# Kernel tuning notes

Measured on AMD Instinct MI355X. Metric: run time of the kernel, lower is better.

## Reference

```python
import jax, jax.numpy as jnp
import numpy as np

B, L, D, H, HD = 2, 8192, 1024, 16, 64
MINI = 64
NC = L // MINI
TTT_BASE_LR = 1.0
NUM_CHUNKS = 4
TEXT_LEN = 64
INIT_OFFSET = 2048


def setup_inputs() -> dict:
    key = jax.random.key(0)
    ks = jax.random.split(key, 16)
    hidden_states = jax.random.normal(ks[0], (B, L, D), dtype=jnp.float32)
    # llama-style rope table as (cos, sin) pairs: [L, HD//2, 2]
    inv_freq = 1.0 / (10000.0 ** (np.arange(0, HD, 2, dtype=np.float32) / HD))
    t = np.arange(L, dtype=np.float32)
    ang = np.outer(t, inv_freq)  # [L, HD//2]
    freqs_cis = jnp.asarray(np.stack([np.cos(ang), np.sin(ang)], axis=-1))
    std = 0.02
    inp = {"hidden_states": hidden_states, "freqs_cis": freqs_cis}
    names = ["wq", "wk", "wv", "wu"]
    for i, n in enumerate(names):
        inp[n + "_w"] = jax.random.normal(ks[1 + i], (D, D), dtype=jnp.float32) * std  # [in, out]
        inp[n + "_b"] = jnp.zeros((D,), dtype=jnp.float32)
    inp["ttt_norm_weight"] = jnp.ones((H, HD), dtype=jnp.float32)
    inp["ttt_norm_bias"] = jnp.zeros((H, HD), dtype=jnp.float32)
    inp["lr_weight"] = jax.random.normal(ks[6], (H, 1, D), dtype=jnp.float32) * std
    inp["lr_bias"] = jnp.zeros((H, 1), dtype=jnp.float32)
    return inp


def _l2norm(x):
    return x / jnp.maximum(jnp.linalg.norm(x, axis=-1, keepdims=True), 1e-12)


def _rope(x, cos, sin):
    # x: [B, L, H, HD]; cos/sin: [L, HD//2] -> broadcast [1, L, 1, HD//2]
    c = cos[None, :, None, :]
    s = sin[None, :, None, :]
    xr, xi = x[..., 0::2], x[..., 1::2]
    out_r = xr * c - xi * s
    out_i = xr * s + xi * c
    return jnp.stack([out_r, out_i], axis=-1).reshape(x.shape)


def _interleave(x):
    # x: [B, H, NC, C, F]; splice text chunks into video scenes (static offsets)
    b, h, nc, c, f = x.shape
    xf = x.reshape(b, h, nc * c, f)
    stl = TEXT_LEN * NUM_CHUNKS
    x_text = xf[:, :, :stl]
    x_video = xf[:, :, stl:]
    texts = jnp.split(x_text, NUM_CHUNKS, axis=2)
    vio = INIT_OFFSET - TEXT_LEN
    vids = [x_video[:, :, :vio]] + list(jnp.split(x_video[:, :, vio:], NUM_CHUNKS - 1, axis=2))
    pieces = [jnp.concatenate([texts[i], vids[i]], axis=2) for i in range(NUM_CHUNKS)]
    return jnp.concatenate(pieces, axis=2).reshape(b, h, nc, c, f)


def reference(hidden_states, freqs_cis, wq_w, wq_b, wk_w, wk_b, wv_w, wv_b,
              wu_w, wu_b, ttt_norm_weight, ttt_norm_bias, lr_weight, lr_bias):
    X = hidden_states  # [B, L, D]
    XQ = (X @ wq_w + wq_b).reshape(B, L, H, HD)
    XK = (X @ wk_w + wk_b).reshape(B, L, H, HD)
    XV = (X @ wv_w + wv_b).reshape(B, L, H, HD)
    XU = (X @ wu_w + wu_b).reshape(B, L, H, HD)

    XQ, XK, XU = _l2norm(XQ), _l2norm(XK), _l2norm(XU)

    # seq_text_length = 0 in process_input -> rope over the whole sequence
    cos, sin = freqs_cis[..., 0], freqs_cis[..., 1]
    XQ = _rope(XQ, cos, sin)
    XK = _rope(XK, cos, sin)
    XU = _rope(XU, cos, sin)

    # ln reconstruction target (std uses Bessel correction like torch.std)
    diff = XV - XK
    mean = diff.mean(axis=-1, keepdims=True)
    std = jnp.std(diff, axis=-1, keepdims=True, ddof=1)
    norm = (diff - mean) / (std + 1e-8)
    XV = ttt_norm_weight[None, None] * norm + ttt_norm_bias[None, None] + XK

    # reshape to mini-batches: [B, H, NC, C, HD]
    def to_mb(t):
        return t.transpose(0, 2, 1, 3).reshape(B, H, NC, MINI, HD)
    XQ, XK, XV, XU = to_mb(XQ), to_mb(XK), to_mb(XV), to_mb(XU)
    Xmb = X.reshape(B, NC, MINI, D)

    # per-head LR gating
    ttt_lr = jnp.einsum('bnkc,hdc->bhnkd', Xmb, lr_weight) + lr_bias.reshape(1, -1, 1, 1, 1)
    ttt_lr = jax.nn.sigmoid(ttt_lr).transpose(0, 1, 2, 4, 3)  # [B, H, NC, 1, C]
    ttt_lr = TTT_BASE_LR * ttt_lr / HD
    eta = (1.0 / MINI) * jnp.tile(ttt_lr, (1, 1, 1, MINI, 1))  # [B, H, NC, C, C]

    XQ, XK, XV, XU = _interleave(XQ), _interleave(XK), _interleave(XV), _interleave(XU)
    eta = _interleave(eta)

    # HD == MINI == 64 so all five stack cleanly
    return jnp.stack([XQ, XK, XV, XU, eta], axis=0)
```

## Files before the change

kernel.cpp:

```cpp
#include <hip/hip_runtime.h>

typedef unsigned int u32;
typedef unsigned short u16;
typedef short short8v __attribute__((ext_vector_type(8)));
typedef float f32x4 __attribute__((ext_vector_type(4)));

#define ND 1024
#define NH 16
#define OUT_T ((size_t)16777216)

#define SBAR() __builtin_amdgcn_s_barrier()
#define VMW(n) asm volatile("s_waitcnt vmcnt(" #n ")" ::: "memory")
#define LGKM0() asm volatile("s_waitcnt lgkmcnt(0)" ::: "memory")

__device__ __forceinline__ u16 f2bf(float f) {
  u32 u = __float_as_uint(f);
  u32 r = u + 0x7fffu + ((u >> 16) & 1u);
  return (u16)(r >> 16);
}

__device__ __forceinline__ short8v pack8(float4 a, float4 b) {
  short8v v;
  v[0] = (short)f2bf(a.x); v[1] = (short)f2bf(a.y);
  v[2] = (short)f2bf(a.z); v[3] = (short)f2bf(a.w);
  v[4] = (short)f2bf(b.x); v[5] = (short)f2bf(b.y);
  v[6] = (short)f2bf(b.z); v[7] = (short)f2bf(b.w);
  return v;
}

__device__ __forceinline__ void gload16(const void* g, void* l) {
  __builtin_amdgcn_global_load_lds((const __attribute__((address_space(1))) void*)g,
                                   (__attribute__((address_space(3))) void*)l, 16, 0, 0);
}

__global__ void k_wt(const float* __restrict__ w0, const float* __restrict__ w1,
                     const float* __restrict__ w2, const float* __restrict__ w3,
                     u16* __restrict__ WT) {
  __shared__ float T[64][65];
  int bid = blockIdx.x;
  int w = bid >> 8;
  int tk = (bid >> 4) & 15, tc = bid & 15;
  const float* W = w == 0 ? w0 : w == 1 ? w1 : w == 2 ? w2 : w3;
  int k0 = tk << 6, c0 = tc << 6;
  int tid = threadIdx.x;
  for (int it = 0; it < 16; ++it) {
    int idx = it * 256 + tid;
    int kk = idx >> 6, cc = idx & 63;
    T[kk][cc] = W[(size_t)(k0 + kk) * ND + c0 + cc];
  }
  __syncthreads();
  for (int it = 0; it < 2; ++it) {
    int ci = it * 256 + tid;
    int cc = ci >> 3, k8 = ci & 7;
    short8v v;
    for (int j = 0; j < 8; ++j) v[j] = (short)f2bf(T[k8 * 8 + j][cc]);
    size_t off = ((((size_t)(w * 16 + tc) * 128) + (tk << 3) + k8) * 64 + cc) * 8;
    *(short8v*)(WT + off) = v;
  }
}

__global__ void k_xbf(const float* __restrict__ X, u16* __restrict__ Xb) {
  size_t i = ((size_t)blockIdx.x * 256 + threadIdx.x) * 8;
  float4 a = *(const float4*)(X + i), b = *(const float4*)(X + i + 4);
  *(short8v*)(Xb + i) = pack8(a, b);
}

__global__ __launch_bounds__(256) void k_lr2(const u16* __restrict__ Xb,
                                             const float* __restrict__ LW,
                                             const float* __restrict__ LB,
                                             float* __restrict__ out) {
  __shared__ __align__(16) char smem[46080];
  u16* LWs = (u16*)smem;
  u16* As = (u16*)(smem + 32768);
  float* El = (float*)(smem + 40960);
  const int tid = threadIdx.x, lane = tid & 63, wid = tid >> 6;
  const int l15 = lane & 15, lg = lane >> 4;
  const int n = blockIdx.x;
  const int tok0 = n << 6;

  {
    int row = tid >> 4;
    int cbase = (tid & 15) << 3;
    const float* src = LW + row * ND + (cbase << 3);
    for (int i = 0; i < 8; ++i) {
      float4 a = *(const float4*)(src + i * 8);
      float4 b = *(const float4*)(src + i * 8 + 4);
      int sc = (cbase + i) ^ (row & 7);
      *(short8v*)(LWs + row * 1024 + (sc << 3)) = pack8(a, b);
    }
  }

  const int arow0 = (wid << 4) + (lane >> 3);
  const u16* asrc = Xb + (size_t)(tok0 + arow0) * ND + ((((lane & 7) ^ arow0) & 7) << 3);
  const u32 aldo = wid << 10;
  const int aoff = ((wid << 4) + l15) << 6;
  const int key = l15 & 7;

  f32x4 acc;
  for (int r = 0; r < 4; ++r) acc[r] = 0.f;
  __syncthreads();

  for (int kt = 0; kt < 16; ++kt) {
    gload16(asrc + (kt << 6), As + aldo);
    gload16(asrc + (kt << 6) + 8 * ND, As + aldo + 512);
    __syncthreads();
    for (int ks = 0; ks < 2; ++ks) {
      int kcl = (ks << 2) + lg;
      int kcg = (kt << 3) + kcl;
      short8v af = *(const short8v*)(As + aoff + ((kcl ^ key) << 3));
      short8v bf = *(const short8v*)(LWs + (l15 << 10) + ((kcg ^ key) << 3));
      acc = __builtin_amdgcn_mfma_f32_16x16x32_bf16(af, bf, acc, 0, 0, 0);
    }
    __syncthreads();
  }

  for (int rr = 0; rr < 4; ++rr) {
    float v = acc[rr] + LB[l15];
    float e = (1.f / (1.f + expf(-v))) * (1.f / 4096.f);
    El[l15 * 72 + (wid << 4) + (lg << 2) + rr] = e;
  }
  __syncthreads();

  const int b = n >> 7, nl = n & 127;
  int q, rc;
  if (nl < 4) { q = nl; rc = 0; }
  else { q = (nl - 4) / 31; rc = nl - 3 - 31 * q; }
  const int pc = q * 32 + rc;
  const int j = tid >> 2, kq = tid & 3;
  size_t base = 4 * OUT_T + (((size_t)(b * NH) << 13) + (pc << 6)) * 64 + (size_t)j * 64;
  for (int h = 0; h < 16; ++h) {
    float* po = out + base + ((size_t)h << 19);
    for (int qq = 0; qq < 4; ++qq) {
      int k0 = (kq + (qq << 2)) << 2;
      const float* ep = El + h * 72 + k0;
      f32x4 t; t[0] = ep[0]; t[1] = ep[1]; t[2] = ep[2]; t[3] = ep[3];
      *(f32x4*)(po + k0) = t;
    }
  }
}

__global__ __launch_bounds__(256, 2) void k_main(
    const u16* __restrict__ Xb, const float* __restrict__ FC,
    const u16* __restrict__ WT,
    const float* __restrict__ qb, const float* __restrict__ kb,
    const float* __restrict__ vb, const float* __restrict__ ub,
    const float* __restrict__ tw, const float* __restrict__ tb,
    float* __restrict__ out) {
  __shared__ __align__(16) char smem[33536];
  float* Cs = (float*)smem;

  const int tid = threadIdx.x;
  const int lane = tid & 63;
  const int w = tid >> 6;
  const int l15 = lane & 15, lg = lane >> 4;
  const int xcd = blockIdx.x & 7;
  const int local = blockIdx.x >> 3;
  const int h = (xcd << 1) | (local >> 7);
  const int s0 = (local & 127) << 7;

  f32x4 acc[8][4];
  for (int i = 0; i < 8; ++i)
    for (int j = 0; j < 4; ++j)
      for (int r = 0; r < 4; ++r) acc[i][j][r] = 0.f;

  const float* bp = (w == 0) ? qb : (w == 1) ? kb : (w == 2) ? vb : ub;
  float biasv[4];
  for (int fn = 0; fn < 4; ++fn) biasv[fn] = bp[h * 64 + fn * 16 + l15];

  const int rS = (w << 5) + (lane >> 2);
  const int chp = lane & 3;
  const u16* asrc = Xb + (size_t)(s0 + rS) * ND + ((chp ^ ((rS >> 1) & 3)) << 3);
  const u32 aldo = w << 10;

  const u16* Bg = WT + (((size_t)(w * 16 + h)) << 16) + (lg << 9) + (l15 << 3);

  int aoff[8], akey[8];
  for (int f = 0; f < 8; ++f) {
    int ra = (f << 4) + l15;
    aoff[f] = ra << 5; akey[f] = (ra >> 1) & 3;
  }

#define STAGE_A(t) do { \
    u16* ad = (u16*)smem + (((t) & 3) << 12); \
    gload16(asrc + ((t) << 5), ad + aldo); \
    gload16(asrc + ((t) << 5) + 16 * ND, ad + aldo + 512); \
  } while (0)

#define LOAD_B(dst, t) do { \
    const u16* bb = Bg + ((t) << 11); \
    dst[0] = *(const short8v*)(bb); \
    dst[1] = *(const short8v*)(bb + 128); \
    dst[2] = *(const short8v*)(bb + 256); \
    dst[3] = *(const short8v*)(bb + 384); \
  } while (0)

#define READ_A(af, t) do { \
    const u16* As_ = (const u16*)smem + (((t) & 3) << 12); \
    _Pragma("unroll") \
    for (int f = 0; f < 8; ++f) \
      af[f] = *(const short8v*)(As_ + aoff[f] + ((lg ^ akey[f]) << 3)); \
  } while (0)

#define MFMA16(af, bv, ofs) do { \
    __builtin_amdgcn_s_setprio(1); \
    _Pragma("unroll") \
    for (int fm = 0; fm < 8; ++fm) { \
      acc[fm][0] = __builtin_amdgcn_mfma_f32_16x16x32_bf16(af[fm], bv[0], acc[fm][0], 0, 0, 0); \
      acc[fm][1] = __builtin_amdgcn_mfma_f32_16x16x32_bf16(af[fm], bv[1], acc[fm][1], 0, 0, 0); \
      acc[fm][2] = __builtin_amdgcn_mfma_f32_16x16x32_bf16(af[fm], bv[2], acc[fm][2], 0, 0, 0); \
      acc[fm][3] = __builtin_amdgcn_mfma_f32_16x16x32_bf16(af[fm], bv[3], acc[fm][3], 0, 0, 0); \
    } \
    __builtin_amdgcn_s_setprio(0); \
  } while (0)

  STAGE_A(0);
  STAGE_A(1);
  short8v b0[4], b1[4];
  LOAD_B(b0, 0);
  VMW(4);
  SBAR();

  short8v af[8];
  for (int kt2 = 0; kt2 < 16; ++kt2) {
    const int e = kt2 << 1;
    READ_A(af, e);
    if (e < 30) STAGE_A(e + 2);
    LOAD_B(b1, e + 1);
    MFMA16(af, b0, e);
    VMW(6);
    SBAR();
    READ_A(af, e + 1);
    if (e + 1 < 30) STAGE_A(e + 3);
    if (e + 1 < 31) LOAD_B(b0, e + 2);
    MFMA16(af, b1, e + 1);
    if (e + 1 < 31) {
      VMW(6);
      SBAR();
    }
  }
  LGKM0();
  SBAR();

#pragma unroll
  for (int ph = 0; ph < 8; ++ph) {
    for (int fn = 0; fn < 4; ++fn)
      for (int rr = 0; rr < 4; ++rr) {
        int rl = (lg << 2) + rr;
        int col = (w << 6) + (fn << 4) + l15;
        Cs[rl * 261 + col] = acc[ph][fn][rr] + biasv[fn];
      }
    LGKM0();
    SBAR();
    {
      int tloc = tid >> 4, o = tid & 15;
      int dbase = o << 2;
      int stok = s0 + (ph << 4) + tloc;
      int b = stok >> 13, seq = stok & 8191;
      const float* crow = Cs + tloc * 261;
      f32x4 fc = *(const f32x4*)(FC + ((size_t)seq << 6) + dbase);
      f32x4 vq = *(const f32x4*)(crow + dbase);
      f32x4 vk = *(const f32x4*)(crow + 64 + dbase);
      f32x4 vv = *(const f32x4*)(crow + 128 + dbase);
      f32x4 vu = *(const f32x4*)(crow + 192 + dbase);
      float sq = 0.f, sk = 0.f, su = 0.f;
      for (int j = 0; j < 4; ++j) {
        sq += vq[j] * vq[j]; sk += vk[j] * vk[j]; su += vu[j] * vu[j];
      }
      sq += __shfl_xor(sq, 1); sq += __shfl_xor(sq, 2);
      sq += __shfl_xor(sq, 4); sq += __shfl_xor(sq, 8);
      sk += __shfl_xor(sk, 1); sk += __shfl_xor(sk, 2);
      sk += __shfl_xor(sk, 4); sk += __shfl_xor(sk, 8);
      su += __shfl_xor(su, 1); su += __shfl_xor(su, 2);
      su += __shfl_xor(su, 4); su += __shfl_xor(su, 8);
      float qi = 1.f / fmaxf(sqrtf(sq), 1e-12f);
      float ki = 1.f / fmaxf(sqrtf(sk), 1e-12f);
      float ui = 1.f / fmaxf(sqrtf(su), 1e-12f);
      int p;
      if (seq < 256) p = ((seq >> 6) << 11) + (seq & 63);
      else { int v = seq - 256; int qc = v / 1984; p = (qc << 11) + 64 + (v - qc * 1984); }
      float* po = out + ((((size_t)(b * NH + h) << 13) + p) << 6) + dbase;
      f32x4 kr;
      kr[0] = vk[0] * ki * fc[0] - vk[1] * ki * fc[1];
      kr[1] = vk[0] * ki * fc[1] + vk[1] * ki * fc[0];
      kr[2] = vk[2] * ki * fc[2] - vk[3] * ki * fc[3];
      kr[3] = vk[2] * ki * fc[3] + vk[3] * ki * fc[2];
      *(f32x4*)(po + OUT_T) = kr;
      f32x4 df;
      float sd = 0.f, sdd = 0.f;
      for (int j = 0; j < 4; ++j) {
        df[j] = vv[j] - kr[j];
        sd += df[j]; sdd += df[j] * df[j];
      }
      sd += __shfl_xor(sd, 1); sd += __shfl_xor(sd, 2);
      sd += __shfl_xor(sd, 4); sd += __shfl_xor(sd, 8);
      sdd += __shfl_xor(sdd, 1); sdd += __shfl_xor(sdd, 2);
      sdd += __shfl_xor(sdd, 4); sdd += __shfl_xor(sdd, 8);
      float mean = sd * (1.f / 64.f);
      float var = (sdd - sd * sd * (1.f / 64.f)) * (1.f / 63.f);
      float istd = 1.f / (sqrtf(fmaxf(var, 0.f)) + 1e-8f);
      f32x4 twv = *(const f32x4*)(tw + h * 64 + dbase);
      f32x4 tbv = *(const f32x4*)(tb + h * 64 + dbase);
      f32x4 vo;
      for (int j = 0; j < 4; ++j)
        vo[j] = twv[j] * ((df[j] - mean) * istd) + tbv[j] + kr[j];
      *(f32x4*)(po + 2 * OUT_T) = vo;
      f32x4 qr;
      qr[0] = vq[0] * qi * fc[0] - vq[1] * qi * fc[1];
      qr[1] = vq[0] * qi * fc[1] + vq[1] * qi * fc[0];
      qr[2] = vq[2] * qi * fc[2] - vq[3] * qi * fc[3];
      qr[3] = vq[2] * qi * fc[3] + vq[3] * qi * fc[2];
      *(f32x4*)po = qr;
      qr[0] = vu[0] * ui * fc[0] - vu[1] * ui * fc[1];
      qr[1] = vu[0] * ui * fc[1] + vu[1] * ui * fc[0];
      qr[2] = vu[2] * ui * fc[2] - vu[3] * ui * fc[3];
      qr[3] = vu[2] * ui * fc[3] + vu[3] * ui * fc[2];
      *(f32x4*)(po + 3 * OUT_T) = qr;
    }
    LGKM0();
    SBAR();
  }
}

extern "C" void kernel_launch(void* const* d_in, const int* in_sizes, int n_in,
                              void* d_out, int out_size, void* d_ws, size_t ws_size,
                              hipStream_t stream) {
  const float* X  = (const float*)d_in[0];
  const float* FC = (const float*)d_in[1];
  const float* wq = (const float*)d_in[2];
  const float* qb = (const float*)d_in[3];
  const float* wk = (const float*)d_in[4];
  const float* kb = (const float*)d_in[5];
  const float* wv = (const float*)d_in[6];
  const float* vb = (const float*)d_in[7];
  const float* wu = (const float*)d_in[8];
  const float* ub = (const float*)d_in[9];
  const float* tw = (const float*)d_in[10];
  const float* tb = (const float*)d_in[11];
  const float* lw = (const float*)d_in[12];
  const float* lb = (const float*)d_in[13];
  float* out = (float*)d_out;
  u16* WT = (u16*)d_ws;
  u16* Xb = (u16*)((char*)d_ws + (8u << 20));

  hipLaunchKernelGGL(k_wt, dim3(1024), dim3(256), 0, stream, wq, wk, wv, wu, WT);
  hipLaunchKernelGGL(k_xbf, dim3(8192), dim3(256), 0, stream, X, Xb);
  hipLaunchKernelGGL(k_lr2, dim3(256), dim3(256), 0, stream, Xb, lw, lb, out);
  hipLaunchKernelGGL(k_main, dim3(2048), dim3(256), 0, stream,
                     Xb, FC, WT, qb, kb, vb, ub, tw, tb, out);
}
```

Baseline: 240.0 us.

## Load A fragments directly from global into registers, dropping LDS staging

Replaces the LDS-staged, swizzled A-tile pipeline (async global-to-LDS loads with manual waitcnt and barriers) with direct per-wave global loads into registers, double-buffered in registers for both A and B. It also remaps blocks so adjacent blocks alternate heads rather than sequence tiles, and shrinks shared memory to just the epilogue buffer. The goal is to remove LDS traffic and barriers from the main loop and improve occupancy. The trade-off is that all four waves now load the same A rows redundantly from global/L2, and the loads are uncoalesced 16-byte row reads, which raises memory traffic.

Measured after the change: 337.0 us. 1.4x slower.

```diff
diff --git a/kernel.cpp b/kernel.cpp
--- a/kernel.cpp
+++ b/kernel.cpp
@@ -8,10 +8,6 @@
 #define ND 1024
 #define NH 16
 #define OUT_T ((size_t)16777216)
-
-#define SBAR() __builtin_amdgcn_s_barrier()
-#define VMW(n) asm volatile("s_waitcnt vmcnt(" #n ")" ::: "memory")
-#define LGKM0() asm volatile("s_waitcnt lgkmcnt(0)" ::: "memory")
 
 __device__ __forceinline__ u16 f2bf(float f) {
   u32 u = __float_as_uint(f);
@@ -146,7 +142,7 @@
     const float* __restrict__ vb, const float* __restrict__ ub,
     const float* __restrict__ tw, const float* __restrict__ tb,
     float* __restrict__ out) {
-  __shared__ __align__(16) char smem[33536];
+  __shared__ __align__(16) char smem[16896];
   float* Cs = (float*)smem;
 
   const int tid = threadIdx.x;
@@ -155,8 +151,8 @@
   const int l15 = lane & 15, lg = lane >> 4;
   const int xcd = blockIdx.x & 7;
   const int local = blockIdx.x >> 3;
-  const int h = (xcd << 1) | (local >> 7);
-  const int s0 = (local & 127) << 7;
+  const int h = (xcd << 1) | (local & 1);
+  const int s0 = (local >> 1) << 7;
 
   f32x4 acc[8][4];
   for (int i = 0; i < 8; ++i)
@@ -167,79 +163,51 @@
   float biasv[4];
   for (int fn = 0; fn < 4; ++fn) biasv[fn] = bp[h * 64 + fn * 16 + l15];
 
-  const int rS = (w << 5) + (lane >> 2);
-  const int chp = lane & 3;
-  const u16* asrc = Xb + (size_t)(s0 + rS) * ND + ((chp ^ ((rS >> 1) & 3)) << 3);
-  const u32 aldo = w << 10;
-
-  const u16* Bg = WT + (((size_t)(w * 16 + h)) << 16) + (lg << 9) + (l15 << 3);
-
-  int aoff[8], akey[8];
-  for (int f = 0; f < 8; ++f) {
-    int ra = (f << 4) + l15;
-    aoff[f] = ra << 5; akey[f] = (ra >> 1) & 3;
-  }
-
-#define STAGE_A(t) do { \
-    u16* ad = (u16*)smem + (((t) & 3) << 12); \
-    gload16(asrc + ((t) << 5), ad + aldo); \
-    gload16(asrc + ((t) << 5) + 16 * ND, ad + aldo + 512); \
+  const u16* ap = Xb + (size_t)(s0 + l15) * ND + (lg << 3);
+  const u16* bq = WT + (((size_t)(w * 16 + h)) << 16) + (lg << 9) + (l15 << 3);
+
+#define LOAD_A(dst, kt) do { \
+    _Pragma("unroll") \
+    for (int f = 0; f < 8; ++f) \
+      dst[f] = *(const short8v*)(ap + (size_t)f * (16 * ND) + ((kt) << 5)); \
   } while (0)
 
-#define LOAD_B(dst, t) do { \
-    const u16* bb = Bg + ((t) << 11); \
+#define LOAD_B(dst, kt) do { \
+    const u16* bb = bq + ((kt) << 11); \
     dst[0] = *(const short8v*)(bb); \
     dst[1] = *(const short8v*)(bb + 128); \
     dst[2] = *(const short8v*)(bb + 256); \
     dst[3] = *(const short8v*)(bb + 384); \
   } while (0)
 
-#define READ_A(af, t) do { \
-    const u16* As_ = (const u16*)smem + (((t) & 3) << 12); \
-    _Pragma("unroll") \
-    for (int f = 0; f < 8; ++f) \
-      af[f] = *(const short8v*)(As_ + aoff[f] + ((lg ^ akey[f]) << 3)); \
-  } while (0)
-
-#define MFMA16(af, bv, ofs) do { \
+#define MFMA32(af, bf) do { \
     __builtin_amdgcn_s_setprio(1); \
     _Pragma("unroll") \
     for (int fm = 0; fm < 8; ++fm) { \
-      acc[fm][0] = __builtin_amdgcn_mfma_f32_16x16x32_bf16(af[fm], bv[0], acc[fm][0], 0, 0, 0); \
-      acc[fm][1] = __builtin_amdgcn_mfma_f32_16x16x32_bf16(af[fm], bv[1], acc[fm][1], 0, 0, 0); \
-      acc[fm][2] = __builtin_amdgcn_mfma_f32_16x16x32_bf16(af[fm], bv[2], acc[fm][2], 0, 0, 0); \
-      acc[fm][3] = __builtin_amdgcn_mfma_f32_16x16x32_bf16(af[fm], bv[3], acc[fm][3], 0, 0, 0); \
+      acc[fm][0] = __builtin_amdgcn_mfma_f32_16x16x32_bf16(af[fm], bf[0], acc[fm][0], 0, 0, 0); \
+      acc[fm][1] = __builtin_amdgcn_mfma_f32_16x16x32_bf16(af[fm], bf[1], acc[fm][1], 0, 0, 0); \
+      acc[fm][2] = __builtin_amdgcn_mfma_f32_16x16x32_bf16(af[fm], bf[2], acc[fm][2], 0, 0, 0); \
+      acc[fm][3] = __builtin_amdgcn_mfma_f32_16x16x32_bf16(af[fm], bf[3], acc[fm][3], 0, 0, 0); \
     } \
     __builtin_amdgcn_s_setprio(0); \
   } while (0)
 
-  STAGE_A(0);
-  STAGE_A(1);
-  short8v b0[4], b1[4];
-  LOAD_B(b0, 0);
-  VMW(4);
-  SBAR();
-
-  short8v af[8];
+  short8v afE[8], afO[8], bfE[4], bfO[4];
+  LOAD_A(afE, 0);
+  LOAD_B(bfE, 0);
   for (int kt2 = 0; kt2 < 16; ++kt2) {
     const int e = kt2 << 1;
-    READ_A(af, e);
-    if (e < 30) STAGE_A(e + 2);
-    LOAD_B(b1, e + 1);
-    MFMA16(af, b0, e);
-    VMW(6);
-    SBAR();
-    READ_A(af, e + 1);
-    if (e + 1 < 30) STAGE_A(e + 3);
-    if (e + 1 < 31) LOAD_B(b0, e + 2);
-    MFMA16(af, b1, e + 1);
-    if (e + 1 < 31) {
-      VMW(6);
-      SBAR();
-    }
-  }
-  LGKM0();
-  SBAR();
+    LOAD_A(afO, e + 1);
+    LOAD_B(bfO, e + 1);
+    MFMA32(afE, bfE);
+    if (e + 2 < 32) {
+      LOAD_A(afE, e + 2);
+      LOAD_B(bfE, e + 2);
+    }
+    MFMA32(afO, bfO);
+  }
+
+  __syncthreads();
 
 #pragma unroll
   for (int ph = 0; ph < 8; ++ph) {
@@ -249,8 +217,7 @@
         int col = (w << 6) + (fn << 4) + l15;
         Cs[rl * 261 + col] = acc[ph][fn][rr] + biasv[fn];
       }
-    LGKM0();
-    SBAR();
+    __syncthreads();
     {
       int tloc = tid >> 4, o = tid & 15;
       int dbase = o << 2;
@@ -316,8 +283,7 @@
       qr[3] = vu[2] * ui * fc[3] + vu[3] * ui * fc[2];
       *(f32x4*)(po + 3 * OUT_T) = qr;
     }
-    LGKM0();
-    SBAR();
+    __syncthreads();
   }
 }
 
```
